# Performance work log

Hardware: AMD Instinct MI355X
Metric: run time of the kernel (lower is better)

## Reference

```python
import jax, jax.numpy as jnp
import numpy as np

KSIZE = 3  # module init kwarg


def setup_inputs() -> dict:
    key = jax.random.key(0)
    k1, k2, k3 = jax.random.split(key, 3)
    shape = (16, 3, 512, 512)  # [B, C, H, W]
    return {
        "sr": jax.random.normal(k1, shape, jnp.float32),
        "sr_ema": jax.random.normal(k2, shape, jnp.float32),
        "hr": jax.random.normal(k3, shape, jnp.float32),
    }


def _local_var(res, ksize):
    """Unbiased variance over a ksize x ksize sliding window with reflect pad.

    Matches torch: reflect-pad then unfold + var(unbiased=True). Implemented as a
    box-filter over sum and sum-of-squares (no ksize^2-larger unfold tensor).
    res: [B, 1, H, W] -> [B, 1, H, W]
    """
    pad = (ksize - 1) // 2
    rp = jnp.pad(res, ((0, 0), (0, 0), (pad, pad), (pad, pad)), mode="reflect")
    n = ksize * ksize
    win = (1, 1, ksize, ksize)
    strides = (1, 1, 1, 1)
    zero = jnp.zeros((), rp.dtype)
    s = jax.lax.reduce_window(rp, zero, jax.lax.add, win, strides, "VALID")
    sq = jax.lax.reduce_window(rp * rp, zero, jax.lax.add, win, strides, "VALID")
    # unbiased: (sum(x^2) - sum(x)^2/n) / (n-1)
    return (sq - s * s / n) / (n - 1)


def reference(sr, sr_ema, hr):
    # per-pixel channel-summed residuals, [B, 1, H, W]
    residual_ema = jnp.sum(jnp.abs(hr - sr_ema), axis=1, keepdims=True) / 255.0
    residual_sr = jnp.sum(jnp.abs(hr - sr), axis=1, keepdims=True) / 255.0

    r_det = jax.lax.stop_gradient(residual_sr)  # .clone().detach() in torch

    # patch-level weight: unbiased var over (C=1, H, W) per sample, ** (1/5)
    n_patch = r_det.shape[1] * r_det.shape[2] * r_det.shape[3]
    mean = jnp.mean(r_det, axis=(-1, -2, -3), keepdims=True)
    patch_var = jnp.sum((r_det - mean) ** 2, axis=(-1, -2, -3), keepdims=True) / (n_patch - 1)
    patch_w = patch_var ** 0.2  # [B,1,1,1]

    pixel_w = _local_var(r_det, KSIZE)  # [B,1,H,W]

    overall_w = patch_w * pixel_w
    overall_w = jnp.where(residual_sr < residual_ema, jnp.zeros((), overall_w.dtype), overall_w)

    # L1 loss (mean reduction) between weighted sr and weighted hr
    return jnp.mean(jnp.abs(overall_w * sr - overall_w * hr))
```

## Files before the change

### kernel.cpp

```cpp
#include <hip/hip_runtime.h>
#include <math.h>


#define BB 16
#define HH 512
#define WW 512
#define HW (HH * WW)
#define CHW (3 * HW)
#define TILE_H 8
#define TILES_PER_BATCH 128
#define NBLOCKS (BB * TILES_PER_BATCH)
#define LDS_STRIDE 264

__device__ __forceinline__ int reflect_h(int gh) {
  gh = gh < 0 ? -gh : gh;
  return gh >= HH ? 2 * HH - 2 - gh : gh;
}

__global__ __launch_bounds__(256) void wl1_main(
    const float* __restrict__ sr, const float* __restrict__ srema,
    const float* __restrict__ hr,
    float* __restrict__ p_sum, float* __restrict__ p_sum2,
    float* __restrict__ p_loss) {
  __shared__ float rt[TILE_H + 2][LDS_STRIDE];
  const int bid = blockIdx.x;
  const int b = bid >> 7;
  const int t = bid & 127;
  const int h0 = (t >> 1) << 3;
  const int w0 = (t & 1) << 8;
  const int tid = threadIdx.x;
  const int c4 = tid & 63;
  const int rs = tid >> 6;
  const float* __restrict__ srb = sr + (size_t)b * CHW;
  const float* __restrict__ hrb = hr + (size_t)b * CHW;
  const float* __restrict__ eb = srema + (size_t)b * CHW;

#pragma unroll
  for (int it = 0; it < 3; ++it) {
    int row = it * 4 + rs;
    if (row < TILE_H + 2) {
      int gh = reflect_h(h0 - 1 + row);
      const float* hb = hrb + gh * WW + w0 + 4 * c4;
      const float* sb = srb + gh * WW + w0 + 4 * c4;
      float4 ha = *(const float4*)(hb);
      float4 hbv = *(const float4*)(hb + HW);
      float4 hc = *(const float4*)(hb + 2 * HW);
      float4 sa = *(const float4*)(sb);
      float4 sbv = *(const float4*)(sb + HW);
      float4 sc = *(const float4*)(sb + 2 * HW);
      float4 r4;
      r4.x = (fabsf(ha.x - sa.x) + fabsf(hbv.x - sbv.x) + fabsf(hc.x - sc.x)) / 255.0f;
      r4.y = (fabsf(ha.y - sa.y) + fabsf(hbv.y - sbv.y) + fabsf(hc.y - sc.y)) / 255.0f;
      r4.z = (fabsf(ha.z - sa.z) + fabsf(hbv.z - sbv.z) + fabsf(hc.z - sc.z)) / 255.0f;
      r4.w = (fabsf(ha.w - sa.w) + fabsf(hbv.w - sbv.w) + fabsf(hc.w - sc.w)) / 255.0f;
      *(float4*)&rt[row][4 + 4 * c4] = r4;
    }
  }
  if (tid < 2 * (TILE_H + 2)) {
    int row = tid >> 1, side = tid & 1;
    int gh = reflect_h(h0 - 1 + row);
    int gw = side ? w0 + 256 : w0 - 1;
    if (gw < 0) gw = 1;
    if (gw > 511) gw = 1022 - gw;
    int base = gh * WW + gw;
    float v = (fabsf(hrb[base] - srb[base]) +
               fabsf(hrb[base + HW] - srb[base + HW]) +
               fabsf(hrb[base + 2 * HW] - srb[base + 2 * HW])) /
              255.0f;
    rt[row][side ? 260 : 3] = v;
  }
  __syncthreads();

  float v1 = 0.f, v2 = 0.f, v3 = 0.f;
#pragma unroll
  for (int rr = 0; rr < 2; ++rr) {
    const int o = rr * 4 + rs;
    float cs[6] = {0, 0, 0, 0, 0, 0}, cq[6] = {0, 0, 0, 0, 0, 0};
    float center[4];
#pragma unroll
    for (int dr = 0; dr < 3; ++dr) {
      const float* lp = &rt[o + dr][4 * c4];
      float4 a = *(const float4*)(lp);
      float4 bq = *(const float4*)(lp + 4);
      float4 cq4 = *(const float4*)(lp + 8);
      float f3 = a.w, f4 = bq.x, f5 = bq.y, f6 = bq.z, f7 = bq.w, f8 = cq4.x;
      cs[0] += f3; cq[0] += f3 * f3;
      cs[1] += f4; cq[1] += f4 * f4;
      cs[2] += f5; cq[2] += f5 * f5;
      cs[3] += f6; cq[3] += f6 * f6;
      cs[4] += f7; cq[4] += f7 * f7;
      cs[5] += f8; cq[5] += f8 * f8;
      if (dr == 1) { center[0] = f4; center[1] = f5; center[2] = f6; center[3] = f7; }
    }
    const int gbase = (h0 + o) * WW + w0 + 4 * c4;
    float4 ha = *(const float4*)(hrb + gbase);
    float4 hb2 = *(const float4*)(hrb + gbase + HW);
    float4 hc = *(const float4*)(hrb + gbase + 2 * HW);
    float4 ea = *(const float4*)(eb + gbase);
    float4 eb2 = *(const float4*)(eb + gbase + HW);
    float4 ec = *(const float4*)(eb + gbase + 2 * HW);
    float e4[4];
    e4[0] = (fabsf(ha.x - ea.x) + fabsf(hb2.x - eb2.x) + fabsf(hc.x - ec.x)) / 255.0f;
    e4[1] = (fabsf(ha.y - ea.y) + fabsf(hb2.y - eb2.y) + fabsf(hc.y - ec.y)) / 255.0f;
    e4[2] = (fabsf(ha.z - ea.z) + fabsf(hb2.z - eb2.z) + fabsf(hc.z - ec.z)) / 255.0f;
    e4[3] = (fabsf(ha.w - ea.w) + fabsf(hb2.w - eb2.w) + fabsf(hc.w - ec.w)) / 255.0f;
#pragma unroll
    for (int cc = 0; cc < 4; ++cc) {
      float s = cs[cc] + cs[cc + 1] + cs[cc + 2];
      float q = cq[cc] + cq[cc + 1] + cq[cc + 2];
      float pvar = (q - s * s / 9.0f) / 8.0f;
      float rc = center[cc];
      v1 += rc;
      v2 += rc * rc;
      if (rc >= e4[cc]) v3 += pvar * (255.0f * rc);
    }
  }

#pragma unroll
  for (int off = 32; off > 0; off >>= 1) {
    v1 += __shfl_down(v1, off, 64);
    v2 += __shfl_down(v2, off, 64);
    v3 += __shfl_down(v3, off, 64);
  }
  __shared__ float red[3][4];
  if (c4 == 0) {
    red[0][rs] = v1;
    red[1][rs] = v2;
    red[2][rs] = v3;
  }
  __syncthreads();
  if (tid == 0) {
    p_sum[bid] = red[0][0] + red[0][1] + red[0][2] + red[0][3];
    p_sum2[bid] = red[1][0] + red[1][1] + red[1][2] + red[1][3];
    p_loss[bid] = red[2][0] + red[2][1] + red[2][2] + red[2][3];
  }
}

__global__ __launch_bounds__(1024) void wl1_reduce(
    const float* __restrict__ p_sum, const float* __restrict__ p_sum2,
    const float* __restrict__ p_loss, float* __restrict__ out) {
  const int tid = threadIdx.x;
  const int b = tid >> 6, k = tid & 63;
  const int i = b * TILES_PER_BATCH + k;
  double s = (double)p_sum[i] + (double)p_sum[i + 64];
  double s2 = (double)p_sum2[i] + (double)p_sum2[i + 64];
  double sl = (double)p_loss[i] + (double)p_loss[i + 64];
#pragma unroll
  for (int off = 32; off > 0; off >>= 1) {
    s += __shfl_down(s, off, 64);
    s2 += __shfl_down(s2, off, 64);
    sl += __shfl_down(sl, off, 64);
  }
  __shared__ double acc[BB];
  if (k == 0) {
    const double n = (double)HW;
    double var = (s2 - s * s / n) / (n - 1.0);
    acc[b] = pow(var, 0.2) * sl;
  }
  __syncthreads();
  if (tid == 0) {
    double tot = 0.0;
#pragma unroll
    for (int j = 0; j < BB; ++j) tot += acc[j];
    out[0] = (float)(tot / (double)((size_t)BB * CHW));
  }
}

extern "C" void kernel_launch(void* const* d_in, const int* in_sizes, int n_in,
                              void* d_out, int out_size, void* d_ws,
                              size_t ws_size, hipStream_t stream) {
  const float* sr = (const float*)d_in[0];
  const float* srema = (const float*)d_in[1];
  const float* hr = (const float*)d_in[2];
  float* out = (float*)d_out;

  float* p_sum = (float*)d_ws;
  float* p_sum2 = p_sum + NBLOCKS;
  float* p_loss = p_sum2 + NBLOCKS;

  wl1_main<<<NBLOCKS, 256, 0, stream>>>(sr, srema, hr, p_sum, p_sum2, p_loss);
  wl1_reduce<<<1, 1024, 0, stream>>>(p_sum, p_sum2, p_loss, out);
}
```

Measured before the change: 159.5 us.

## Split into streaming residual pass and stencil pass over a sign-encoded residual field

Restructures the fused kernel into two passes. The first streams sr, sr_ema and hr once, computes the residual, folds the ema mask into its sign, writes one float field, and reduces sum and sum-of-squares. The second runs the 3x3 local-variance stencil on that single-channel field instead of re-reading 6-channel inputs with halo rows. This removes the roughly 25% halo over-read of the raw inputs, at the cost of a 16 MB intermediate write plus read and one extra launch.

```diff
diff --git a/kernel.cpp b/kernel.cpp
--- a/kernel.cpp
+++ b/kernel.cpp
@@ -7,9 +7,9 @@
 #define WW 512
 #define HW (HH * WW)
 #define CHW (3 * HW)
-#define TILE_H 8
-#define TILES_PER_BATCH 128
-#define NBLOCKS (BB * TILES_PER_BATCH)
+
+#define NB1 2048
+#define NB2 2048
 #define LDS_STRIDE 264
 
 __device__ __forceinline__ int reflect_h(int gh) {
@@ -17,12 +17,95 @@
   return gh >= HH ? 2 * HH - 2 - gh : gh;
 }
 
-__global__ __launch_bounds__(256) void wl1_main(
+__global__ __launch_bounds__(256) void wl1_stream(
     const float* __restrict__ sr, const float* __restrict__ srema,
-    const float* __restrict__ hr,
-    float* __restrict__ p_sum, float* __restrict__ p_sum2,
-    float* __restrict__ p_loss) {
-  __shared__ float rt[TILE_H + 2][LDS_STRIDE];
+    const float* __restrict__ hr, float* __restrict__ rfield,
+    float* __restrict__ p_sum, float* __restrict__ p_sum2) {
+  const int tid = threadIdx.x;
+  const int bid = blockIdx.x;
+  const int b = bid >> 7;
+  const int rem = ((bid & 127) << 9) + (tid << 1);
+  const size_t base = (size_t)b * CHW + ((size_t)rem << 2);
+  const float* __restrict__ hp = hr + base;
+  const float* __restrict__ sp = sr + base;
+  const float* __restrict__ ep = srema + base;
+
+  float4 h0a = *(const float4*)(hp);
+  float4 h0b = *(const float4*)(hp + 4);
+  float4 h1a = *(const float4*)(hp + HW);
+  float4 h1b = *(const float4*)(hp + HW + 4);
+  float4 h2a = *(const float4*)(hp + 2 * HW);
+  float4 h2b = *(const float4*)(hp + 2 * HW + 4);
+  float4 s0a = *(const float4*)(sp);
+  float4 s0b = *(const float4*)(sp + 4);
+  float4 s1a = *(const float4*)(sp + HW);
+  float4 s1b = *(const float4*)(sp + HW + 4);
+  float4 s2a = *(const float4*)(sp + 2 * HW);
+  float4 s2b = *(const float4*)(sp + 2 * HW + 4);
+  float4 e0a = *(const float4*)(ep);
+  float4 e0b = *(const float4*)(ep + 4);
+  float4 e1a = *(const float4*)(ep + HW);
+  float4 e1b = *(const float4*)(ep + HW + 4);
+  float4 e2a = *(const float4*)(ep + 2 * HW);
+  float4 e2b = *(const float4*)(ep + 2 * HW + 4);
+
+  float4 ra, rb, ea, eb2;
+  ra.x = (fabsf(h0a.x - s0a.x) + fabsf(h1a.x - s1a.x) + fabsf(h2a.x - s2a.x)) / 255.0f;
+  ra.y = (fabsf(h0a.y - s0a.y) + fabsf(h1a.y - s1a.y) + fabsf(h2a.y - s2a.y)) / 255.0f;
+  ra.z = (fabsf(h0a.z - s0a.z) + fabsf(h1a.z - s1a.z) + fabsf(h2a.z - s2a.z)) / 255.0f;
+  ra.w = (fabsf(h0a.w - s0a.w) + fabsf(h1a.w - s1a.w) + fabsf(h2a.w - s2a.w)) / 255.0f;
+  rb.x = (fabsf(h0b.x - s0b.x) + fabsf(h1b.x - s1b.x) + fabsf(h2b.x - s2b.x)) / 255.0f;
+  rb.y = (fabsf(h0b.y - s0b.y) + fabsf(h1b.y - s1b.y) + fabsf(h2b.y - s2b.y)) / 255.0f;
+  rb.z = (fabsf(h0b.z - s0b.z) + fabsf(h1b.z - s1b.z) + fabsf(h2b.z - s2b.z)) / 255.0f;
+  rb.w = (fabsf(h0b.w - s0b.w) + fabsf(h1b.w - s1b.w) + fabsf(h2b.w - s2b.w)) / 255.0f;
+  ea.x = (fabsf(h0a.x - e0a.x) + fabsf(h1a.x - e1a.x) + fabsf(h2a.x - e2a.x)) / 255.0f;
+  ea.y = (fabsf(h0a.y - e0a.y) + fabsf(h1a.y - e1a.y) + fabsf(h2a.y - e2a.y)) / 255.0f;
+  ea.z = (fabsf(h0a.z - e0a.z) + fabsf(h1a.z - e1a.z) + fabsf(h2a.z - e2a.z)) / 255.0f;
+  ea.w = (fabsf(h0a.w - e0a.w) + fabsf(h1a.w - e1a.w) + fabsf(h2a.w - e2a.w)) / 255.0f;
+  eb2.x = (fabsf(h0b.x - e0b.x) + fabsf(h1b.x - e1b.x) + fabsf(h2b.x - e2b.x)) / 255.0f;
+  eb2.y = (fabsf(h0b.y - e0b.y) + fabsf(h1b.y - e1b.y) + fabsf(h2b.y - e2b.y)) / 255.0f;
+  eb2.z = (fabsf(h0b.z - e0b.z) + fabsf(h1b.z - e1b.z) + fabsf(h2b.z - e2b.z)) / 255.0f;
+  eb2.w = (fabsf(h0b.w - e0b.w) + fabsf(h1b.w - e1b.w) + fabsf(h2b.w - e2b.w)) / 255.0f;
+
+  float4 ma, mb;
+  ma.x = (ra.x >= ea.x) ? ra.x : -ra.x;
+  ma.y = (ra.y >= ea.y) ? ra.y : -ra.y;
+  ma.z = (ra.z >= ea.z) ? ra.z : -ra.z;
+  ma.w = (ra.w >= ea.w) ? ra.w : -ra.w;
+  mb.x = (rb.x >= eb2.x) ? rb.x : -rb.x;
+  mb.y = (rb.y >= eb2.y) ? rb.y : -rb.y;
+  mb.z = (rb.z >= eb2.z) ? rb.z : -rb.z;
+  mb.w = (rb.w >= eb2.w) ? rb.w : -rb.w;
+
+  float* __restrict__ rf = rfield + (((size_t)b << 18) + ((size_t)rem << 2));
+  *(float4*)(rf) = ma;
+  *(float4*)(rf + 4) = mb;
+
+  float v1 = ra.x + ra.y + ra.z + ra.w + rb.x + rb.y + rb.z + rb.w;
+  float v2 = ra.x * ra.x + ra.y * ra.y + ra.z * ra.z + ra.w * ra.w +
+             rb.x * rb.x + rb.y * rb.y + rb.z * rb.z + rb.w * rb.w;
+
+#pragma unroll
+  for (int off = 32; off > 0; off >>= 1) {
+    v1 += __shfl_down(v1, off, 64);
+    v2 += __shfl_down(v2, off, 64);
+  }
+  __shared__ float red[2][4];
+  const int wv = tid >> 6;
+  if ((tid & 63) == 0) {
+    red[0][wv] = v1;
+    red[1][wv] = v2;
+  }
+  __syncthreads();
+  if (tid == 0) {
+    p_sum[bid] = red[0][0] + red[0][1] + red[0][2] + red[0][3];
+    p_sum2[bid] = red[1][0] + red[1][1] + red[1][2] + red[1][3];
+  }
+}
+
+__global__ __launch_bounds__(256) void wl1_var(
+    const float* __restrict__ rfield, float* __restrict__ p_loss) {
+  __shared__ float rt[10][LDS_STRIDE];
   const int bid = blockIdx.x;
   const int b = bid >> 7;
   const int t = bid & 127;
@@ -31,117 +114,74 @@
   const int tid = threadIdx.x;
   const int c4 = tid & 63;
   const int rs = tid >> 6;
-  const float* __restrict__ srb = sr + (size_t)b * CHW;
-  const float* __restrict__ hrb = hr + (size_t)b * CHW;
-  const float* __restrict__ eb = srema + (size_t)b * CHW;
+  const float* __restrict__ rb = rfield + ((size_t)b << 18);
 
 #pragma unroll
   for (int it = 0; it < 3; ++it) {
     int row = it * 4 + rs;
-    if (row < TILE_H + 2) {
+    if (row < 10) {
       int gh = reflect_h(h0 - 1 + row);
-      const float* hb = hrb + gh * WW + w0 + 4 * c4;
-      const float* sb = srb + gh * WW + w0 + 4 * c4;
-      float4 ha = *(const float4*)(hb);
-      float4 hbv = *(const float4*)(hb + HW);
-      float4 hc = *(const float4*)(hb + 2 * HW);
-      float4 sa = *(const float4*)(sb);
-      float4 sbv = *(const float4*)(sb + HW);
-      float4 sc = *(const float4*)(sb + 2 * HW);
-      float4 r4;
-      r4.x = (fabsf(ha.x - sa.x) + fabsf(hbv.x - sbv.x) + fabsf(hc.x - sc.x)) / 255.0f;
-      r4.y = (fabsf(ha.y - sa.y) + fabsf(hbv.y - sbv.y) + fabsf(hc.y - sc.y)) / 255.0f;
-      r4.z = (fabsf(ha.z - sa.z) + fabsf(hbv.z - sbv.z) + fabsf(hc.z - sc.z)) / 255.0f;
-      r4.w = (fabsf(ha.w - sa.w) + fabsf(hbv.w - sbv.w) + fabsf(hc.w - sc.w)) / 255.0f;
-      *(float4*)&rt[row][4 + 4 * c4] = r4;
+      float4 v = *(const float4*)(rb + gh * WW + w0 + 4 * c4);
+      *(float4*)&rt[row][4 + 4 * c4] = v;
     }
   }
-  if (tid < 2 * (TILE_H + 2)) {
+  if (tid < 20) {
     int row = tid >> 1, side = tid & 1;
     int gh = reflect_h(h0 - 1 + row);
     int gw = side ? w0 + 256 : w0 - 1;
     if (gw < 0) gw = 1;
     if (gw > 511) gw = 1022 - gw;
-    int base = gh * WW + gw;
-    float v = (fabsf(hrb[base] - srb[base]) +
-               fabsf(hrb[base + HW] - srb[base + HW]) +
-               fabsf(hrb[base + 2 * HW] - srb[base + 2 * HW])) /
-              255.0f;
-    rt[row][side ? 260 : 3] = v;
-  }
-  __syncthreads();
-
-  float v1 = 0.f, v2 = 0.f, v3 = 0.f;
+    rt[row][side ? 260 : 3] = rb[gh * WW + gw];
+  }
+  __syncthreads();
+
+  float v3 = 0.f;
 #pragma unroll
   for (int rr = 0; rr < 2; ++rr) {
     const int o = rr * 4 + rs;
     float cs[6] = {0, 0, 0, 0, 0, 0}, cq[6] = {0, 0, 0, 0, 0, 0};
-    float center[4];
+    float craw[4];
 #pragma unroll
     for (int dr = 0; dr < 3; ++dr) {
       const float* lp = &rt[o + dr][4 * c4];
       float4 a = *(const float4*)(lp);
       float4 bq = *(const float4*)(lp + 4);
       float4 cq4 = *(const float4*)(lp + 8);
-      float f3 = a.w, f4 = bq.x, f5 = bq.y, f6 = bq.z, f7 = bq.w, f8 = cq4.x;
+      float f3 = fabsf(a.w), f4 = fabsf(bq.x), f5 = fabsf(bq.y),
+            f6 = fabsf(bq.z), f7 = fabsf(bq.w), f8 = fabsf(cq4.x);
       cs[0] += f3; cq[0] += f3 * f3;
       cs[1] += f4; cq[1] += f4 * f4;
       cs[2] += f5; cq[2] += f5 * f5;
       cs[3] += f6; cq[3] += f6 * f6;
       cs[4] += f7; cq[4] += f7 * f7;
       cs[5] += f8; cq[5] += f8 * f8;
-      if (dr == 1) { center[0] = f4; center[1] = f5; center[2] = f6; center[3] = f7; }
+      if (dr == 1) { craw[0] = bq.x; craw[1] = bq.y; craw[2] = bq.z; craw[3] = bq.w; }
     }
-    const int gbase = (h0 + o) * WW + w0 + 4 * c4;
-    float4 ha = *(const float4*)(hrb + gbase);
-    float4 hb2 = *(const float4*)(hrb + gbase + HW);
-    float4 hc = *(const float4*)(hrb + gbase + 2 * HW);
-    float4 ea = *(const float4*)(eb + gbase);
-    float4 eb2 = *(const float4*)(eb + gbase + HW);
-    float4 ec = *(const float4*)(eb + gbase + 2 * HW);
-    float e4[4];
-    e4[0] = (fabsf(ha.x - ea.x) + fabsf(hb2.x - eb2.x) + fabsf(hc.x - ec.x)) / 255.0f;
-    e4[1] = (fabsf(ha.y - ea.y) + fabsf(hb2.y - eb2.y) + fabsf(hc.y - ec.y)) / 255.0f;
-    e4[2] = (fabsf(ha.z - ea.z) + fabsf(hb2.z - eb2.z) + fabsf(hc.z - ec.z)) / 255.0f;
-    e4[3] = (fabsf(ha.w - ea.w) + fabsf(hb2.w - eb2.w) + fabsf(hc.w - ec.w)) / 255.0f;
 #pragma unroll
     for (int cc = 0; cc < 4; ++cc) {
       float s = cs[cc] + cs[cc + 1] + cs[cc + 2];
       float q = cq[cc] + cq[cc + 1] + cq[cc + 2];
       float pvar = (q - s * s / 9.0f) / 8.0f;
-      float rc = center[cc];
-      v1 += rc;
-      v2 += rc * rc;
-      if (rc >= e4[cc]) v3 += pvar * (255.0f * rc);
+      float raw = craw[cc];
+      float rc = fabsf(raw);
+      if (raw >= 0.0f) v3 += pvar * (255.0f * rc);
     }
   }
 
 #pragma unroll
-  for (int off = 32; off > 0; off >>= 1) {
-    v1 += __shfl_down(v1, off, 64);
-    v2 += __shfl_down(v2, off, 64);
-    v3 += __shfl_down(v3, off, 64);
-  }
-  __shared__ float red[3][4];
-  if (c4 == 0) {
-    red[0][rs] = v1;
-    red[1][rs] = v2;
-    red[2][rs] = v3;
-  }
-  __syncthreads();
-  if (tid == 0) {
-    p_sum[bid] = red[0][0] + red[0][1] + red[0][2] + red[0][3];
-    p_sum2[bid] = red[1][0] + red[1][1] + red[1][2] + red[1][3];
-    p_loss[bid] = red[2][0] + red[2][1] + red[2][2] + red[2][3];
-  }
-}
-
-__global__ __launch_bounds__(1024) void wl1_reduce(
+  for (int off = 32; off > 0; off >>= 1) v3 += __shfl_down(v3, off, 64);
+  __shared__ float red[4];
+  if (c4 == 0) red[rs] = v3;
+  __syncthreads();
+  if (tid == 0) p_loss[bid] = red[0] + red[1] + red[2] + red[3];
+}
+
+__global__ __launch_bounds__(1024) void wl1_final(
     const float* __restrict__ p_sum, const float* __restrict__ p_sum2,
     const float* __restrict__ p_loss, float* __restrict__ out) {
   const int tid = threadIdx.x;
   const int b = tid >> 6, k = tid & 63;
-  const int i = b * TILES_PER_BATCH + k;
+  const int i = b * 128 + k;
   double s = (double)p_sum[i] + (double)p_sum[i + 64];
   double s2 = (double)p_sum2[i] + (double)p_sum2[i + 64];
   double sl = (double)p_loss[i] + (double)p_loss[i + 64];
@@ -175,9 +215,11 @@
   float* out = (float*)d_out;
 
   float* p_sum = (float*)d_ws;
-  float* p_sum2 = p_sum + NBLOCKS;
-  float* p_loss = p_sum2 + NBLOCKS;
-
-  wl1_main<<<NBLOCKS, 256, 0, stream>>>(sr, srema, hr, p_sum, p_sum2, p_loss);
-  wl1_reduce<<<1, 1024, 0, stream>>>(p_sum, p_sum2, p_loss, out);
-}
+  float* p_sum2 = p_sum + NB1;
+  float* p_loss = p_sum2 + NB1;
+  float* rfield = p_loss + NB2;
+
+  wl1_stream<<<NB1, 256, 0, stream>>>(sr, srema, hr, rfield, p_sum, p_sum2);
+  wl1_var<<<NB2, 256, 0, stream>>>(rfield, p_loss);
+  wl1_final<<<1, 1024, 0, stream>>>(p_sum, p_sum2, p_loss, out);
+}
```

Result: slower. 164.1 us (+2.9%).
